# Optimization experiments

Hardware: AMD Instinct MI355X
Metric: run time of the kernel (lower is better)

The kernel has to match this reference:

```python
import jax, jax.numpy as jnp
import numpy as np
import math

B, T, D = 2, 2048, 1024
H, HD = 16, 64
MAX_LEN = 2048


def _build_rope_sin_cos(max_seq, head_dim):
    inv_freq = 1.0 / 10000 ** (jnp.arange(0, head_dim, 2) / head_dim)
    positions = jnp.arange(max_seq)
    sinusoid_inp = jnp.einsum('i,j->ij', positions.astype(jnp.float32), inv_freq.astype(jnp.float32))
    sin = jnp.repeat(jnp.sin(sinusoid_inp), 2, axis=-1)
    cos = jnp.repeat(jnp.cos(sinusoid_inp), 2, axis=-1)
    return sin, cos


def _rotate_half(x):
    x1 = x[..., ::2]
    x2 = x[..., 1::2]
    return jnp.stack((-x2, x1), axis=-1).reshape(x.shape)


def setup_inputs() -> dict:
    key = jax.random.key(0)
    ks = jax.random.split(key, 6)
    x = jax.random.normal(ks[0], (B, T, D), dtype=jnp.float32)
    # causal boolean mask (B, T, T)
    mask = jnp.broadcast_to(jnp.tril(jnp.ones((T, T), dtype=bool)), (B, T, T))
    s = 1.0 / math.sqrt(D)
    wq = jax.random.normal(ks[1], (D, H, HD), dtype=jnp.float32) * s
    wk = jax.random.normal(ks[2], (D, H, HD), dtype=jnp.float32) * s
    wv = jax.random.normal(ks[3], (D, H, HD), dtype=jnp.float32) * s
    wo = jax.random.normal(ks[4], (H * HD, D), dtype=jnp.float32) * (1.0 / math.sqrt(H * HD))
    return {"x": x, "mask": mask, "wq": wq, "wk": wk, "wv": wv, "wo": wo}


def reference(x, mask, wq, wk, wv, wo):
    Bx, Tx, Dx = x.shape
    # q/k/v projections: DenseGeneral D -> (H, HD)
    q = jnp.einsum('btd,dhe->bthe', x, wq)
    k = jnp.einsum('btd,dhe->bthe', x, wk)
    v = jnp.einsum('btd,dhe->bthe', x, wv)
    sin, cos = _build_rope_sin_cos(MAX_LEN, HD)
    sin_t = sin[:Tx][None, :, None, :]
    cos_t = cos[:Tx][None, :, None, :]
    q = q * cos_t + _rotate_half(q) * sin_t
    k = k * cos_t + _rotate_half(k) * sin_t
    q = jnp.transpose(q, (0, 2, 1, 3))  # (B,H,T,HD)
    k = jnp.transpose(k, (0, 2, 1, 3))
    v = jnp.transpose(v, (0, 2, 1, 3))
    scale = 1.0 / math.sqrt(HD)
    logits = jnp.einsum('bhqd,bhkd->bhqk', q, k) * scale
    mask_f = mask[:, None, :, :].astype(jnp.float32)
    logits = logits + (1.0 - mask_f) * -1e10
    w = jax.nn.softmax(logits, axis=-1)
    attn_out = jnp.einsum('bhqk,bhkd->bhqd', w, v)
    attn_out = jnp.transpose(attn_out, (0, 2, 1, 3)).reshape(Bx, Tx, -1)
    return attn_out @ wo
```

## Files before the change

### kernel.cpp

```cpp
#include <hip/hip_runtime.h>
#include <cstdint>
#include <cstddef>

typedef __bf16 bf16x8 __attribute__((ext_vector_type(8)));
typedef __bf16 bf16x2 __attribute__((ext_vector_type(2)));
typedef float f32x4 __attribute__((ext_vector_type(4)));
typedef float f32x16 __attribute__((ext_vector_type(16)));
typedef unsigned int u32x4 __attribute__((ext_vector_type(4)));
#define UNROLL _Pragma("unroll")

__device__ __forceinline__ unsigned short f2bf(float f) {
  unsigned int x = __builtin_bit_cast(unsigned int, f);
  x += 0x7fffu + ((x >> 16) & 1u);
  return (unsigned short)(x >> 16);
}
__device__ __forceinline__ float bf2f(unsigned short u) {
  return __builtin_bit_cast(float, (unsigned int)u << 16);
}
__device__ __forceinline__ unsigned int cvtpk(float a, float b) {
  bf16x2 t; t[0] = (__bf16)a; t[1] = (__bf16)b;
  return __builtin_bit_cast(unsigned int, t);
}
__device__ __forceinline__ void async16(const void* g, void* l) {
  __builtin_amdgcn_global_load_lds((void __attribute__((address_space(1)))*)g,
                                   (void __attribute__((address_space(3)))*)l,
                                   16, 0, 0);
}

__global__ void prep_x(const float* __restrict__ x, unsigned short* __restrict__ xb) {
  int i = blockIdx.x * 256 + threadIdx.x;
  const float4* p = (const float4*)(x + (size_t)i * 8);
  float4 a = p[0], b = p[1];
  ushort4 o0 = {f2bf(a.x), f2bf(a.y), f2bf(a.z), f2bf(a.w)};
  ushort4 o1 = {f2bf(b.x), f2bf(b.y), f2bf(b.z), f2bf(b.w)};
  ushort4* q = (ushort4*)(xb + (size_t)i * 8);
  q[0] = o0; q[1] = o1;
}

__global__ void prep_w(const float* __restrict__ wq, const float* __restrict__ wk,
                       const float* __restrict__ wv, const float* __restrict__ wo,
                       unsigned short* __restrict__ out) {
  __shared__ float tile[32][33];
  const float* src = blockIdx.z == 0 ? wq : blockIdx.z == 1 ? wk : blockIdx.z == 2 ? wv : wo;
  unsigned short* dst = out + (size_t)blockIdx.z * 1048576;
  int kb = blockIdx.x * 32, nb = blockIdx.y * 32;
  int c = threadIdx.x & 31, r4 = (threadIdx.x >> 5) * 4;
UNROLL
  for (int i = 0; i < 4; ++i)
    tile[r4 + i][c] = src[(size_t)(kb + r4 + i) * 1024 + nb + c];
  __syncthreads();
UNROLL
  for (int i = 0; i < 4; ++i)
    dst[(size_t)(nb + r4 + i) * 1024 + kb + c] = f2bf(tile[c][r4 + i]);
}

__global__ void prep_rope(float2* __restrict__ tab) {
  int idx = blockIdx.x * 256 + threadIdx.x;
  int t = idx >> 5, i = idx & 31;
  float inv = exp2f(-(float)i * (13.287712379549449f / 32.0f));
  float ang = (float)t * inv;
  tab[idx] = make_float2(cosf(ang), sinf(ang));
}

__global__ __launch_bounds__(256, 3) void gemmqkv(
    const unsigned short* __restrict__ A, const unsigned short* __restrict__ Bt,
    unsigned short* __restrict__ qout, unsigned short* __restrict__ kout,
    unsigned short* __restrict__ vtout, const float2* __restrict__ rope) {
  __shared__ __align__(16) unsigned short As[128 * 64];
  __shared__ __align__(16) unsigned short Bs[128 * 64];
  const int tid = threadIdx.x;
  const int lane = tid & 63, wid = tid >> 6;
  const int wr = wid >> 1, wc = wid & 1;
  const int g = lane >> 4, r16 = lane & 15;
  const int m0 = blockIdx.y * 128, n0 = blockIdx.x * 128;

  f32x4 acc[4][4];
UNROLL
  for (int i = 0; i < 4; ++i)
UNROLL
    for (int j = 0; j < 4; ++j) acc[i][j] = (f32x4){0.f, 0.f, 0.f, 0.f};

  const int ce = (((tid & 7) ^ ((tid >> 3) & 7)) << 3);
  const unsigned short* gA = A + (size_t)(m0 + (tid >> 3)) * 1024 + ce;
  const unsigned short* gB = Bt + (size_t)(n0 + (tid >> 3)) * 1024 + ce;
  char* lA = (char*)As + tid * 16;
  char* lB = (char*)Bs + tid * 16;

  const int swz = (r16 & 7) << 4;

  for (int u = 0; u < 16; ++u) {
    const int k0 = u * 64;
UNROLL
    for (int s = 0; s < 4; ++s) {
      async16(gA + (size_t)s * 32 * 1024 + k0, lA + s * 4096);
      async16(gB + (size_t)s * 32 * 1024 + k0, lB + s * 4096);
    }
    __syncthreads();
UNROLL
    for (int kk = 0; kk < 2; ++kk) {
      bf16x8 af[4], bfr[4];
UNROLL
      for (int mi = 0; mi < 4; ++mi)
        af[mi] = *(const bf16x8*)((const char*)As +
                  (wr * 64 + mi * 16 + r16) * 128 + ((kk * 64 + g * 16) ^ swz));
UNROLL
      for (int ni = 0; ni < 4; ++ni)
        bfr[ni] = *(const bf16x8*)((const char*)Bs +
                  (wc * 64 + ni * 16 + r16) * 128 + ((kk * 64 + g * 16) ^ swz));
UNROLL
      for (int mi = 0; mi < 4; ++mi)
UNROLL
        for (int ni = 0; ni < 4; ++ni)
          acc[mi][ni] = __builtin_amdgcn_mfma_f32_16x16x32_bf16(af[mi], bfr[ni],
                                                                acc[mi][ni], 0, 0, 0);
    }
    __syncthreads();
  }

  const int which = n0 >> 10;
  const int b = (m0 >= 2048) ? 1 : 0;
  const float QSCL = 0.18033688011112042f;
UNROLL
  for (int mi = 0; mi < 4; ++mi) {
    const int rowb = m0 + wr * 64 + mi * 16 + g * 4;
    const int trow = rowb & 2047;
UNROLL
    for (int ni = 0; ni < 4; ++ni) {
      const int n = n0 + wc * 64 + ni * 16 + r16;
      const int h = (n >> 6) & 15, e = n & 63;
      f32x4 v = acc[mi][ni];
      if (which < 2) {
        const int fi = e >> 1;
        const bool ev = (e & 1) == 0;
UNROLL
        for (int j = 0; j < 4; ++j) {
          float2 cs = rope[(trow + j) * 32 + fi];
          float p = __shfl_xor(v[j], 1);
          v[j] = ev ? (v[j] * cs.x - p * cs.y) : (v[j] * cs.x + p * cs.y);
        }
        if (which == 0) { v[0] *= QSCL; v[1] *= QSCL; v[2] *= QSCL; v[3] *= QSCL; }
      }
      if (which == 2) {
        size_t base = (((size_t)b * 16 + h) * 64 + e) * 2048 + trow;
        ushort4 pkv = {f2bf(v[0]), f2bf(v[1]), f2bf(v[2]), f2bf(v[3])};
        *(ushort4*)(vtout + base) = pkv;
      } else {
        unsigned short* dst = (which == 0) ? qout : kout;
        size_t base = (((size_t)b * 16 + h) * 2048 + trow) * 64 + e;
UNROLL
        for (int j = 0; j < 4; ++j) dst[base + (size_t)j * 64] = f2bf(v[j]);
      }
    }
  }
}

__global__ __launch_bounds__(256, 4) void gemm_o(
    const unsigned short* __restrict__ A, const unsigned short* __restrict__ Bt,
    float* __restrict__ out) {
  __shared__ __align__(16) unsigned short As[2][64 * 64];
  __shared__ __align__(16) unsigned short Bs[2][64 * 64];
  const int tid = threadIdx.x;
  const int lane = tid & 63, wid = tid >> 6;
  const int wm = wid >> 1, wn = wid & 1;
  const int g = lane >> 4, r16 = lane & 15;
  const int m0 = blockIdx.y * 64, n0 = blockIdx.x * 64;

  f32x4 acc[2][2];
UNROLL
  for (int i = 0; i < 2; ++i)
UNROLL
    for (int j = 0; j < 2; ++j) acc[i][j] = (f32x4){0.f, 0.f, 0.f, 0.f};

  const int ce = (((tid & 7) ^ ((tid >> 3) & 7)) << 3);
  const unsigned short* gA = A + (size_t)(m0 + (tid >> 3)) * 1024 + ce;
  const unsigned short* gB = Bt + (size_t)(n0 + (tid >> 3)) * 1024 + ce;
  const int dst0 = tid * 16;
  const int swz = (r16 & 7) << 4;

#define OSTG(bb, koff) { \
    async16(gA + (koff),             (char*)As[bb] + dst0); \
    async16(gA + 32 * 1024 + (koff), (char*)As[bb] + dst0 + 4096); \
    async16(gB + (koff),             (char*)Bs[bb] + dst0); \
    async16(gB + 32 * 1024 + (koff), (char*)Bs[bb] + dst0 + 4096); }

  OSTG(0, 0)
  for (int u = 0; u < 16; ++u) {
    const int bsel = u & 1;
    if (u + 1 < 16) { OSTG(bsel ^ 1, (u + 1) * 64) }
    __builtin_amdgcn_sched_barrier(0);
    if (u + 1 < 16) { asm volatile("s_waitcnt vmcnt(4)" ::: "memory"); }
    else            { asm volatile("s_waitcnt vmcnt(0)" ::: "memory"); }
    __builtin_amdgcn_s_barrier();
    __builtin_amdgcn_sched_barrier(0);
UNROLL
    for (int kk = 0; kk < 2; ++kk) {
      bf16x8 af[2], bfr[2];
UNROLL
      for (int mi = 0; mi < 2; ++mi)
        af[mi] = *(const bf16x8*)((const char*)As[bsel] +
                  (wm * 32 + mi * 16 + r16) * 128 + ((kk * 64 + g * 16) ^ swz));
UNROLL
      for (int ni = 0; ni < 2; ++ni)
        bfr[ni] = *(const bf16x8*)((const char*)Bs[bsel] +
                  (wn * 32 + ni * 16 + r16) * 128 + ((kk * 64 + g * 16) ^ swz));
UNROLL
      for (int mi = 0; mi < 2; ++mi)
UNROLL
        for (int ni = 0; ni < 2; ++ni)
          acc[mi][ni] = __builtin_amdgcn_mfma_f32_16x16x32_bf16(af[mi], bfr[ni],
                                                                acc[mi][ni], 0, 0, 0);
    }
    __builtin_amdgcn_sched_barrier(0);
    __builtin_amdgcn_s_barrier();
  }
#undef OSTG

UNROLL
  for (int mi = 0; mi < 2; ++mi) {
    const int rowb = m0 + wm * 32 + mi * 16 + g * 4;
UNROLL
    for (int ni = 0; ni < 2; ++ni) {
      const int n = n0 + wn * 32 + ni * 16 + r16;
UNROLL
      for (int j = 0; j < 4; ++j)
        out[(size_t)(rowb + j) * 1024 + n] = acc[mi][ni][j];
    }
  }
}

__device__ const signed char c_qt[32]   = {15,15,10,10,15,14,14,14,13, 9, 9, 4,13,13,12,12, 8, 8,12,11,11,11, 7, 7, 3, 6, 6, 5, 5, 2, 1, 0};
__device__ const signed char c_t0[32]   = { 0,11, 0,11,22, 0,10,20, 0, 0,10, 0,10,19, 0, 9, 0, 9,18, 0, 8,16, 0, 8, 0, 0, 7, 0, 6, 0, 0, 0};
__device__ const signed char c_len[32]  = {11,11,11,11,10,10,10,10,10,10,10,10, 9, 9, 9, 9, 9, 9, 8, 8, 8, 8, 8, 8, 8, 7, 7, 6, 6, 6, 4, 2};
__device__ const signed char c_slot[32] = {24,25,10,11,26,21,22,23,18, 8, 9,-1,19,20,15,16, 6, 7,17,12,13,14, 4, 5,-1, 2, 3, 0, 1,-1,-1,-1};

__global__ __launch_bounds__(256, 4) void attn4(
    const unsigned short* __restrict__ qb, const unsigned short* __restrict__ kb,
    const unsigned short* __restrict__ vtb, unsigned short* __restrict__ attnb,
    unsigned short* __restrict__ po, float* __restrict__ ml) {
  __shared__ __align__(16) char smem[2][16384];
  const int tid = threadIdx.x;
  const int lane = tid & 63, w = tid >> 6;
  const int l31 = lane & 31, h = lane >> 5;
  const int bh = blockIdx.x;
  const int item = blockIdx.y;
  const int qt = c_qt[item];
  const int t0 = c_t0[item];
  const int t1 = t0 + c_len[item];
  const int slot = c_slot[item];
  const int q0w = qt * 128 + w * 32;
  const int qg = q0w + l31;
  const size_t kvbase = (size_t)bh * (2048 * 64);

  bf16x8 qf[4];
  const unsigned short* qp = qb + kvbase + (size_t)qg * 64 + h * 8;
UNROLL
  for (int kk = 0; kk < 4; ++kk) qf[kk] = *(const bf16x8*)(qp + kk * 16);

  u32x4 of; of[0] = of[1] = of[2] = of[3] = 0x3F803F80u;
  const bf16x8 onesf = __builtin_bit_cast(bf16x8, of);

  const int lr = lane >> 3;
  const int cb2 = ((lane & 7) ^ lr) << 3;
  const bool isK = (w < 2);
  const int c0 = isK ? w * 4 : (w - 2) * 4;
  const unsigned short* srcp[4];
  int dstoff[4];
  const size_t step = isK ? 4096 : 64;
UNROLL
  for (int s = 0; s < 4; ++s) {
    int r = (c0 + s) * 8 + lr;
    srcp[s] = isK ? (kb + kvbase + (size_t)r * 64 + cb2)
                  : (vtb + kvbase + (size_t)r * 2048 + cb2);
    dstoff[s] = (w * 4 + s) * 1024 + lane * 16;
  }

  f32x16 o0, o1, lacc;
UNROLL
  for (int r = 0; r < 16; ++r) { o0[r] = 0.f; o1[r] = 0.f; lacc[r] = 0.f; }

UNROLL
  for (int s = 0; s < 4; ++s) async16(srcp[s] + (size_t)t0 * step, &smem[0][0] + dstoff[s]);

  const int swz = (l31 & 7) << 4;
  for (int t = t0; t < t1; ++t) {
    const int kt0 = t << 6;
    if (t + 1 < t1) {
      char* db = &smem[(t + 1 - t0) & 1][0];
UNROLL
      for (int s = 0; s < 4; ++s)
        async16(srcp[s] + (size_t)(t + 1) * step, db + dstoff[s]);
      __builtin_amdgcn_sched_barrier(0);
      asm volatile("s_waitcnt vmcnt(4)" ::: "memory");
    } else {
      __builtin_amdgcn_sched_barrier(0);
      asm volatile("s_waitcnt vmcnt(0)" ::: "memory");
    }
    __builtin_amdgcn_s_barrier();
    __builtin_amdgcn_sched_barrier(0);
    if (kt0 <= q0w + 31) {
      const char* cbuf = &smem[(t - t0) & 1][0];
      f32x16 sa, sb;
UNROLL
      for (int r = 0; r < 16; ++r) { sa[r] = 0.f; sb[r] = 0.f; }
      __builtin_amdgcn_s_setprio(1);
UNROLL
      for (int kk = 0; kk < 4; ++kk) {
        bf16x8 kf = *(const bf16x8*)(cbuf + l31 * 128 + ((kk * 32 + h * 16) ^ swz));
        sa = __builtin_amdgcn_mfma_f32_32x32x16_bf16(kf, qf[kk], sa, 0, 0, 0);
      }
UNROLL
      for (int kk = 0; kk < 4; ++kk) {
        bf16x8 kf = *(const bf16x8*)(cbuf + (32 + l31) * 128 + ((kk * 32 + h * 16) ^ swz));
        sb = __builtin_amdgcn_mfma_f32_32x32x16_bf16(kf, qf[kk], sb, 0, 0, 0);
      }
      __builtin_amdgcn_s_setprio(0);
      if (kt0 + 63 > q0w) {
UNROLL
        for (int r = 0; r < 16; ++r) {
          int koff = (r & 3) + 8 * (r >> 2) + 4 * h;
          if (kt0 + koff > qg) sa[r] = -3e38f;
          if (kt0 + 32 + koff > qg) sb[r] = -3e38f;
        }
      }
UNROLL
      for (int r = 0; r < 16; ++r) {
        sa[r] = exp2f(sa[r]);
        sb[r] = exp2f(sb[r]);
      }
      unsigned int lo[8], hi[8];
UNROLL
      for (int b8 = 0; b8 < 4; ++b8) {
        lo[b8]     = cvtpk(sa[4 * b8], sa[4 * b8 + 1]);
        hi[b8]     = cvtpk(sa[4 * b8 + 2], sa[4 * b8 + 3]);
        lo[4 + b8] = cvtpk(sb[4 * b8], sb[4 * b8 + 1]);
        hi[4 + b8] = cvtpk(sb[4 * b8 + 2], sb[4 * b8 + 3]);
      }
      bf16x8 pa[4];
UNROLL
      for (int j = 0; j < 4; ++j) {
        const int bb = (j >> 1) * 4 + (j & 1) * 2;
        unsigned int a0 = lo[bb], b0 = lo[bb + 1];
        unsigned int a1 = hi[bb], b1 = hi[bb + 1];
        asm volatile("v_permlane32_swap_b32 %0, %1" : "+v"(a0), "+v"(b0));
        asm volatile("v_permlane32_swap_b32 %0, %1" : "+v"(a1), "+v"(b1));
        u32x4 f;
        f[0] = a0; f[1] = a1; f[2] = b0; f[3] = b1;
        pa[j] = __builtin_bit_cast(bf16x8, f);
      }
      __builtin_amdgcn_s_setprio(1);
UNROLL
      for (int j = 0; j < 4; ++j) {
        bf16x8 v0 = *(const bf16x8*)(cbuf + 8192 + l31 * 128 + ((j * 32 + h * 16) ^ swz));
        bf16x8 v1 = *(const bf16x8*)(cbuf + 8192 + (32 + l31) * 128 + ((j * 32 + h * 16) ^ swz));
        o0 = __builtin_amdgcn_mfma_f32_32x32x16_bf16(pa[j], v0, o0, 0, 0, 0);
        o1 = __builtin_amdgcn_mfma_f32_32x32x16_bf16(pa[j], v1, o1, 0, 0, 0);
        lacc = __builtin_amdgcn_mfma_f32_32x32x16_bf16(pa[j], onesf, lacc, 0, 0, 0);
      }
      __builtin_amdgcn_s_setprio(0);
    }
    __builtin_amdgcn_sched_barrier(0);
    __builtin_amdgcn_s_barrier();
  }

  if (slot < 0) {
    const int b = bh >> 4, hh = bh & 15;
UNROLL
    for (int r = 0; r < 16; ++r) {
      const int qg2 = q0w + (r & 3) + 8 * (r >> 2) + 4 * h;
      const size_t base = (((size_t)b * 2048 + qg2) * 16 + hh) * 64 + l31;
      const float iv = 1.0f / lacc[r];
      attnb[base]      = f2bf(o0[r] * iv);
      attnb[base + 32] = f2bf(o1[r] * iv);
    }
  } else {
    const int p = bh * 27 + slot;
    if (l31 == 0) {
UNROLL
      for (int r = 0; r < 16; ++r)
        ml[p * 128 + w * 32 + (r & 3) + 8 * (r >> 2) + 4 * h] = lacc[r];
    }
    unsigned short* pb = po + (size_t)p * 8192;
UNROLL
    for (int r = 0; r < 16; ++r) {
      const int rl = w * 32 + (r & 3) + 8 * (r >> 2) + 4 * h;
      const float iv = 1.0f / lacc[r];
      pb[rl * 64 + l31]      = f2bf(o0[r] * iv);
      pb[rl * 64 + l31 + 32] = f2bf(o1[r] * iv);
    }
  }
}

__global__ void attn_combine(const unsigned short* __restrict__ po,
                             const float* __restrict__ ml,
                             unsigned short* __restrict__ attnb) {
  const int idx = blockIdx.x * 256 + threadIdx.x;
  const int cg = idx & 3;
  const int row = (idx >> 2) & 127;
  const int t2 = idx >> 9;
  const int qi = t2 % 11;
  const int bh = t2 / 11;
  const int qt = qi + 5;
  const int cnt = (qt < 11) ? 2 : 3;
  const int base = (qt < 11) ? (qt - 5) * 2 : 12 + (qt - 11) * 3;
  const int slotg = bh * 27 + base;
  float acc[16];
UNROLL
  for (int i = 0; i < 16; ++i) acc[i] = 0.f;
  float wsum = 0.f;
  for (int i = 0; i < cnt; ++i) {
    const float l = ml[(slotg + i) * 128 + row];
    wsum += l;
    const ushort4* p = (const ushort4*)(po + (size_t)(slotg + i) * 8192 + row * 64 + cg * 16);
UNROLL
    for (int v = 0; v < 4; ++v) {
      ushort4 u = p[v];
      acc[v * 4 + 0] += l * bf2f(u.x);
      acc[v * 4 + 1] += l * bf2f(u.y);
      acc[v * 4 + 2] += l * bf2f(u.z);
      acc[v * 4 + 3] += l * bf2f(u.w);
    }
  }
  const float inv = 1.0f / wsum;
  const int b = bh >> 4, hh = bh & 15;
  const int q = qt * 128 + row;
  ushort4* out = (ushort4*)(attnb + (((size_t)b * 2048 + q) * 16 + hh) * 64 + cg * 16);
UNROLL
  for (int v = 0; v < 4; ++v) {
    ushort4 o;
    o.x = f2bf(acc[v * 4 + 0] * inv);
    o.y = f2bf(acc[v * 4 + 1] * inv);
    o.z = f2bf(acc[v * 4 + 2] * inv);
    o.w = f2bf(acc[v * 4 + 3] * inv);
    out[v] = o;
  }
}

extern "C" void kernel_launch(void* const* d_in, const int* in_sizes, int n_in,
                              void* d_out, int out_size, void* d_ws, size_t ws_size,
                              hipStream_t stream) {
  (void)in_sizes; (void)n_in; (void)out_size; (void)ws_size;
  const float* x = (const float*)d_in[0];
  const float* wq = (const float*)d_in[2];
  const float* wk = (const float*)d_in[3];
  const float* wv = (const float*)d_in[4];
  const float* wo = (const float*)d_in[5];

  unsigned short* xb = (unsigned short*)d_ws;
  unsigned short* wT = xb + 4 * 1024 * 1024;
  float2* rope = (float2*)(wT + 4 * 1024 * 1024);
  unsigned short* qb = (unsigned short*)(rope + 65536);
  unsigned short* kbuf = qb + 4 * 1024 * 1024;
  unsigned short* vtb = kbuf + 4 * 1024 * 1024;
  unsigned short* attnb = vtb + 4 * 1024 * 1024;

  unsigned short* po = xb;
  float* mlb = (float*)rope;

  prep_x<<<dim3(2048), dim3(256), 0, stream>>>(x, xb);
  prep_w<<<dim3(32, 32, 4), dim3(256), 0, stream>>>(wq, wk, wv, wo, wT);
  prep_rope<<<dim3(256), dim3(256), 0, stream>>>(rope);
  gemmqkv<<<dim3(24, 32), dim3(256), 0, stream>>>(xb, wT, qb, kbuf, vtb, rope);
  attn4<<<dim3(32, 32), dim3(256), 0, stream>>>(qb, kbuf, vtb, attnb, po, mlb);
  attn_combine<<<dim3(704), dim3(256), 0, stream>>>(po, mlb, attnb);
  gemm_o<<<dim3(16, 64), dim3(256), 0, stream>>>(attnb, wT + 3 * 1024 * 1024,
                                                 (float*)d_out);
}
```

Before: 111.6 us.

## Fuse prep kernels into one launch and deepen attention K/V pipeline

Merges the three preprocessing kernels (x conversion, weight transpose, rope table) into one launch dispatched by block index, saving two kernel launches. The attention kernel moves from a two-slot to a four-slot LDS ring and processes K/V tiles in pairs per barrier, prefetching two pairs ahead. This halves the barriers per tile and hides more load latency. LDS per block doubles to 64KB and launch bounds drop to 2 blocks/CU, which may reduce occupancy; odd-length ranges issue redundant clamped loads.

```diff
diff --git a/kernel.cpp b/kernel.cpp
--- a/kernel.cpp
+++ b/kernel.cpp
@@ -27,39 +27,43 @@
                                    16, 0, 0);
 }
 
-__global__ void prep_x(const float* __restrict__ x, unsigned short* __restrict__ xb) {
-  int i = blockIdx.x * 256 + threadIdx.x;
-  const float4* p = (const float4*)(x + (size_t)i * 8);
-  float4 a = p[0], b = p[1];
-  ushort4 o0 = {f2bf(a.x), f2bf(a.y), f2bf(a.z), f2bf(a.w)};
-  ushort4 o1 = {f2bf(b.x), f2bf(b.y), f2bf(b.z), f2bf(b.w)};
-  ushort4* q = (ushort4*)(xb + (size_t)i * 8);
-  q[0] = o0; q[1] = o1;
-}
-
-__global__ void prep_w(const float* __restrict__ wq, const float* __restrict__ wk,
-                       const float* __restrict__ wv, const float* __restrict__ wo,
-                       unsigned short* __restrict__ out) {
+__global__ void prep_all(const float* __restrict__ x,
+                         const float* __restrict__ wq, const float* __restrict__ wk,
+                         const float* __restrict__ wv, const float* __restrict__ wo,
+                         unsigned short* __restrict__ xb,
+                         unsigned short* __restrict__ wT,
+                         float2* __restrict__ ropetab) {
   __shared__ float tile[32][33];
-  const float* src = blockIdx.z == 0 ? wq : blockIdx.z == 1 ? wk : blockIdx.z == 2 ? wv : wo;
-  unsigned short* dst = out + (size_t)blockIdx.z * 1048576;
-  int kb = blockIdx.x * 32, nb = blockIdx.y * 32;
-  int c = threadIdx.x & 31, r4 = (threadIdx.x >> 5) * 4;
-UNROLL
-  for (int i = 0; i < 4; ++i)
-    tile[r4 + i][c] = src[(size_t)(kb + r4 + i) * 1024 + nb + c];
-  __syncthreads();
-UNROLL
-  for (int i = 0; i < 4; ++i)
-    dst[(size_t)(nb + r4 + i) * 1024 + kb + c] = f2bf(tile[c][r4 + i]);
-}
-
-__global__ void prep_rope(float2* __restrict__ tab) {
-  int idx = blockIdx.x * 256 + threadIdx.x;
-  int t = idx >> 5, i = idx & 31;
-  float inv = exp2f(-(float)i * (13.287712379549449f / 32.0f));
-  float ang = (float)t * inv;
-  tab[idx] = make_float2(cosf(ang), sinf(ang));
+  const int bx = blockIdx.x, tid = threadIdx.x;
+  if (bx < 2048) {
+    int i = bx * 256 + tid;
+    const float4* p = (const float4*)(x + (size_t)i * 8);
+    float4 a = p[0], b = p[1];
+    ushort4 o0 = {f2bf(a.x), f2bf(a.y), f2bf(a.z), f2bf(a.w)};
+    ushort4 o1 = {f2bf(b.x), f2bf(b.y), f2bf(b.z), f2bf(b.w)};
+    ushort4* q = (ushort4*)(xb + (size_t)i * 8);
+    q[0] = o0; q[1] = o1;
+  } else if (bx < 6144) {
+    const int idx = bx - 2048;
+    const int z = idx >> 10;
+    const float* src = z == 0 ? wq : z == 1 ? wk : z == 2 ? wv : wo;
+    unsigned short* dst = wT + (size_t)z * 1048576;
+    const int kb = (idx & 31) * 32, nb = ((idx >> 5) & 31) * 32;
+    const int c = tid & 31, r4 = (tid >> 5) * 4;
+UNROLL
+    for (int i = 0; i < 4; ++i)
+      tile[r4 + i][c] = src[(size_t)(kb + r4 + i) * 1024 + nb + c];
+    __syncthreads();
+UNROLL
+    for (int i = 0; i < 4; ++i)
+      dst[(size_t)(nb + r4 + i) * 1024 + kb + c] = f2bf(tile[c][r4 + i]);
+  } else {
+    int idx = (bx - 6144) * 256 + tid;
+    int t = idx >> 5, i = idx & 31;
+    float inv = exp2f(-(float)i * (13.287712379549449f / 32.0f));
+    float ang = (float)t * inv;
+    ropetab[idx] = make_float2(cosf(ang), sinf(ang));
+  }
 }
 
 __global__ __launch_bounds__(256, 3) void gemmqkv(
@@ -233,11 +237,11 @@
 __device__ const signed char c_len[32]  = {11,11,11,11,10,10,10,10,10,10,10,10, 9, 9, 9, 9, 9, 9, 8, 8, 8, 8, 8, 8, 8, 7, 7, 6, 6, 6, 4, 2};
 __device__ const signed char c_slot[32] = {24,25,10,11,26,21,22,23,18, 8, 9,-1,19,20,15,16, 6, 7,17,12,13,14, 4, 5,-1, 2, 3, 0, 1,-1,-1,-1};
 
-__global__ __launch_bounds__(256, 4) void attn4(
+__global__ __launch_bounds__(256, 2) void attn4(
     const unsigned short* __restrict__ qb, const unsigned short* __restrict__ kb,
     const unsigned short* __restrict__ vtb, unsigned short* __restrict__ attnb,
     unsigned short* __restrict__ po, float* __restrict__ ml) {
-  __shared__ __align__(16) char smem[2][16384];
+  __shared__ __align__(16) char smem[4][16384];
   const int tid = threadIdx.x;
   const int lane = tid & 63, w = tid >> 6;
   const int l31 = lane & 31, h = lane >> 5;
@@ -278,89 +282,97 @@
 UNROLL
   for (int r = 0; r < 16; ++r) { o0[r] = 0.f; o1[r] = 0.f; lacc[r] = 0.f; }
 
-UNROLL
-  for (int s = 0; s < 4; ++s) async16(srcp[s] + (size_t)t0 * step, &smem[0][0] + dstoff[s]);
+#define STAGE_T(tv, bufv) { \
+    const int tc_ = ((tv) < t1) ? (tv) : (t1 - 1); \
+    char* db_ = &smem[(bufv)][0]; \
+    async16(srcp[0] + (size_t)tc_ * step, db_ + dstoff[0]); \
+    async16(srcp[1] + (size_t)tc_ * step, db_ + dstoff[1]); \
+    async16(srcp[2] + (size_t)tc_ * step, db_ + dstoff[2]); \
+    async16(srcp[3] + (size_t)tc_ * step, db_ + dstoff[3]); }
+
+  const int np = (t1 - t0 + 1) >> 1;
+  STAGE_T(t0, 0) STAGE_T(t0 + 1, 1)
+  if (np > 1) { STAGE_T(t0 + 2, 2) STAGE_T(t0 + 3, 3) }
 
   const int swz = (l31 & 7) << 4;
-  for (int t = t0; t < t1; ++t) {
-    const int kt0 = t << 6;
-    if (t + 1 < t1) {
-      char* db = &smem[(t + 1 - t0) & 1][0];
-UNROLL
-      for (int s = 0; s < 4; ++s)
-        async16(srcp[s] + (size_t)(t + 1) * step, db + dstoff[s]);
-      __builtin_amdgcn_sched_barrier(0);
-      asm volatile("s_waitcnt vmcnt(4)" ::: "memory");
-    } else {
-      __builtin_amdgcn_sched_barrier(0);
-      asm volatile("s_waitcnt vmcnt(0)" ::: "memory");
-    }
+  for (int p = 0; p < np; ++p) {
+    const int tp = t0 + 2 * p;
+    __builtin_amdgcn_sched_barrier(0);
+    if (p + 1 < np) { asm volatile("s_waitcnt vmcnt(8)" ::: "memory"); }
+    else            { asm volatile("s_waitcnt vmcnt(0)" ::: "memory"); }
     __builtin_amdgcn_s_barrier();
     __builtin_amdgcn_sched_barrier(0);
-    if (kt0 <= q0w + 31) {
-      const char* cbuf = &smem[(t - t0) & 1][0];
-      f32x16 sa, sb;
-UNROLL
-      for (int r = 0; r < 16; ++r) { sa[r] = 0.f; sb[r] = 0.f; }
-      __builtin_amdgcn_s_setprio(1);
-UNROLL
-      for (int kk = 0; kk < 4; ++kk) {
-        bf16x8 kf = *(const bf16x8*)(cbuf + l31 * 128 + ((kk * 32 + h * 16) ^ swz));
-        sa = __builtin_amdgcn_mfma_f32_32x32x16_bf16(kf, qf[kk], sa, 0, 0, 0);
+UNROLL
+    for (int sub = 0; sub < 2; ++sub) {
+      const int t = tp + sub;
+      const int kt0 = t << 6;
+      if (t < t1 && kt0 <= q0w + 31) {
+        const char* cbuf = &smem[(2 * p + sub) & 3][0];
+        f32x16 sa, sb;
+UNROLL
+        for (int r = 0; r < 16; ++r) { sa[r] = 0.f; sb[r] = 0.f; }
+        __builtin_amdgcn_s_setprio(1);
+UNROLL
+        for (int kk = 0; kk < 4; ++kk) {
+          bf16x8 kf = *(const bf16x8*)(cbuf + l31 * 128 + ((kk * 32 + h * 16) ^ swz));
+          sa = __builtin_amdgcn_mfma_f32_32x32x16_bf16(kf, qf[kk], sa, 0, 0, 0);
+        }
+UNROLL
+        for (int kk = 0; kk < 4; ++kk) {
+          bf16x8 kf = *(const bf16x8*)(cbuf + (32 + l31) * 128 + ((kk * 32 + h * 16) ^ swz));
+          sb = __builtin_amdgcn_mfma_f32_32x32x16_bf16(kf, qf[kk], sb, 0, 0, 0);
+        }
+        __builtin_amdgcn_s_setprio(0);
+        if (kt0 + 63 > q0w) {
+UNROLL
+          for (int r = 0; r < 16; ++r) {
+            int koff = (r & 3) + 8 * (r >> 2) + 4 * h;
+            if (kt0 + koff > qg) sa[r] = -3e38f;
+            if (kt0 + 32 + koff > qg) sb[r] = -3e38f;
+          }
+        }
+UNROLL
+        for (int r = 0; r < 16; ++r) {
+          sa[r] = exp2f(sa[r]);
+          sb[r] = exp2f(sb[r]);
+        }
+        unsigned int lo[8], hi[8];
+UNROLL
+        for (int b8 = 0; b8 < 4; ++b8) {
+          lo[b8]     = cvtpk(sa[4 * b8], sa[4 * b8 + 1]);
+          hi[b8]     = cvtpk(sa[4 * b8 + 2], sa[4 * b8 + 3]);
+          lo[4 + b8] = cvtpk(sb[4 * b8], sb[4 * b8 + 1]);
+          hi[4 + b8] = cvtpk(sb[4 * b8 + 2], sb[4 * b8 + 3]);
+        }
+        bf16x8 pa[4];
+UNROLL
+        for (int j = 0; j < 4; ++j) {
+          const int bb = (j >> 1) * 4 + (j & 1) * 2;
+          unsigned int a0 = lo[bb], b0 = lo[bb + 1];
+          unsigned int a1 = hi[bb], b1 = hi[bb + 1];
+          asm volatile("v_permlane32_swap_b32 %0, %1" : "+v"(a0), "+v"(b0));
+          asm volatile("v_permlane32_swap_b32 %0, %1" : "+v"(a1), "+v"(b1));
+          u32x4 f;
+          f[0] = a0; f[1] = a1; f[2] = b0; f[3] = b1;
+          pa[j] = __builtin_bit_cast(bf16x8, f);
+        }
+        __builtin_amdgcn_s_setprio(1);
+UNROLL
+        for (int j = 0; j < 4; ++j) {
+          bf16x8 v0 = *(const bf16x8*)(cbuf + 8192 + l31 * 128 + ((j * 32 + h * 16) ^ swz));
+          bf16x8 v1 = *(const bf16x8*)(cbuf + 8192 + (32 + l31) * 128 + ((j * 32 + h * 16) ^ swz));
+          o0 = __builtin_amdgcn_mfma_f32_32x32x16_bf16(pa[j], v0, o0, 0, 0, 0);
+          o1 = __builtin_amdgcn_mfma_f32_32x32x16_bf16(pa[j], v1, o1, 0, 0, 0);
+          lacc = __builtin_amdgcn_mfma_f32_32x32x16_bf16(pa[j], onesf, lacc, 0, 0, 0);
+        }
+        __builtin_amdgcn_s_setprio(0);
       }
-UNROLL
-      for (int kk = 0; kk < 4; ++kk) {
-        bf16x8 kf = *(const bf16x8*)(cbuf + (32 + l31) * 128 + ((kk * 32 + h * 16) ^ swz));
-        sb = __builtin_amdgcn_mfma_f32_32x32x16_bf16(kf, qf[kk], sb, 0, 0, 0);
-      }
-      __builtin_amdgcn_s_setprio(0);
-      if (kt0 + 63 > q0w) {
-UNROLL
-        for (int r = 0; r < 16; ++r) {
-          int koff = (r & 3) + 8 * (r >> 2) + 4 * h;
-          if (kt0 + koff > qg) sa[r] = -3e38f;
-          if (kt0 + 32 + koff > qg) sb[r] = -3e38f;
-        }
-      }
-UNROLL
-      for (int r = 0; r < 16; ++r) {
-        sa[r] = exp2f(sa[r]);
-        sb[r] = exp2f(sb[r]);
-      }
-      unsigned int lo[8], hi[8];
-UNROLL
-      for (int b8 = 0; b8 < 4; ++b8) {
-        lo[b8]     = cvtpk(sa[4 * b8], sa[4 * b8 + 1]);
-        hi[b8]     = cvtpk(sa[4 * b8 + 2], sa[4 * b8 + 3]);
-        lo[4 + b8] = cvtpk(sb[4 * b8], sb[4 * b8 + 1]);
-        hi[4 + b8] = cvtpk(sb[4 * b8 + 2], sb[4 * b8 + 3]);
-      }
-      bf16x8 pa[4];
-UNROLL
-      for (int j = 0; j < 4; ++j) {
-        const int bb = (j >> 1) * 4 + (j & 1) * 2;
-        unsigned int a0 = lo[bb], b0 = lo[bb + 1];
-        unsigned int a1 = hi[bb], b1 = hi[bb + 1];
-        asm volatile("v_permlane32_swap_b32 %0, %1" : "+v"(a0), "+v"(b0));
-        asm volatile("v_permlane32_swap_b32 %0, %1" : "+v"(a1), "+v"(b1));
-        u32x4 f;
-        f[0] = a0; f[1] = a1; f[2] = b0; f[3] = b1;
-        pa[j] = __builtin_bit_cast(bf16x8, f);
-      }
-      __builtin_amdgcn_s_setprio(1);
-UNROLL
-      for (int j = 0; j < 4; ++j) {
-        bf16x8 v0 = *(const bf16x8*)(cbuf + 8192 + l31 * 128 + ((j * 32 + h * 16) ^ swz));
-        bf16x8 v1 = *(const bf16x8*)(cbuf + 8192 + (32 + l31) * 128 + ((j * 32 + h * 16) ^ swz));
-        o0 = __builtin_amdgcn_mfma_f32_32x32x16_bf16(pa[j], v0, o0, 0, 0, 0);
-        o1 = __builtin_amdgcn_mfma_f32_32x32x16_bf16(pa[j], v1, o1, 0, 0, 0);
-        lacc = __builtin_amdgcn_mfma_f32_32x32x16_bf16(pa[j], onesf, lacc, 0, 0, 0);
-      }
-      __builtin_amdgcn_s_setprio(0);
     }
     __builtin_amdgcn_sched_barrier(0);
     __builtin_amdgcn_s_barrier();
-  }
+    if (p + 2 < np) { STAGE_T(tp + 4, (2 * p) & 3) STAGE_T(tp + 5, (2 * p + 1) & 3) }
+  }
+#undef STAGE_T
 
   if (slot < 0) {
     const int b = bh >> 4, hh = bh & 15;
@@ -456,9 +468,7 @@
   unsigned short* po = xb;
   float* mlb = (float*)rope;
 
-  prep_x<<<dim3(2048), dim3(256), 0, stream>>>(x, xb);
-  prep_w<<<dim3(32, 32, 4), dim3(256), 0, stream>>>(wq, wk, wv, wo, wT);
-  prep_rope<<<dim3(256), dim3(256), 0, stream>>>(rope);
+  prep_all<<<dim3(6400), dim3(256), 0, stream>>>(x, wq, wk, wv, wo, xb, wT, rope);
   gemmqkv<<<dim3(24, 32), dim3(256), 0, stream>>>(xb, wT, qb, kbuf, vtb, rope);
   attn4<<<dim3(32, 32), dim3(256), 0, stream>>>(qb, kbuf, vtb, attnb, po, mlb);
   attn_combine<<<dim3(704), dim3(256), 0, stream>>>(po, mlb, attnb);
```

New measurement: 107.6 us. -3.6%, faster.
